# Performance work log

Hardware: AMD Instinct MI355X
Metric: run time of the kernel (lower is better)

Reference implementation:

```python
import jax, jax.numpy as jnp
import numpy as np

B, C, H, W = 64, 512, 7, 7        # x4: dim_b=512, layer4 spatial 7x7
HY, WY = 28, 28                   # y (x1): layer1 56x56 -> cov1 stride2 -> 28x28
NUM_HEADS = 8
HEAD_DIM = C // NUM_HEADS
SCALE = HEAD_DIM ** -0.5
K1, K2 = 2, 3
LN_EPS = 1e-5


def _avgpool_same(y, k, p):
    # torch nn.AvgPool2d(kernel=k, stride=1, padding=p), count_include_pad=True
    s = jax.lax.reduce_window(y, 0.0, jax.lax.add, (1, 1, k, k), (1, 1, 1, 1),
                              [(0, 0), (0, 0), (p, p), (p, p)])
    return s / float(k * k)


def setup_inputs() -> dict:
    key = jax.random.key(0)
    ks = jax.random.split(key, 8)
    x = jax.random.normal(ks[0], (B, C, H, W), dtype=jnp.float32)
    y = jax.random.normal(ks[1], (B, C, HY, WY), dtype=jnp.float32)
    # Linear weights stored as [in, out] (apply via x @ W)
    Wq = jax.random.normal(ks[2], (C, C), dtype=jnp.float32) * 0.02
    Wkv = jax.random.normal(ks[3], (C, 2 * C), dtype=jnp.float32) * 0.02
    Wproj = jax.random.normal(ks[4], (C, C), dtype=jnp.float32) * 0.02
    bproj = jnp.zeros((C,), dtype=jnp.float32)
    gamma = jnp.ones((C,), dtype=jnp.float32)
    beta = jnp.zeros((C,), dtype=jnp.float32)
    attn_w1 = jnp.full((1,), 0.5, dtype=jnp.float32)
    attn_w2 = jnp.full((1,), 0.5, dtype=jnp.float32)
    return dict(x=x, y=y, Wq=Wq, Wkv=Wkv, Wproj=Wproj, bproj=bproj,
                gamma=gamma, beta=beta, attn_w1=attn_w1, attn_w2=attn_w2)


def _topk_masked_softmax(attn, kc):
    # torch: scatter top-kc indices into a 0/1 mask, then where(mask>0, attn, -inf).
    # Equivalent (tie-free, as with continuous random logits): keep entries >= kth value.
    thr = jax.lax.top_k(attn, kc)[0][..., -1:]
    masked = jnp.where(attn >= jax.lax.stop_gradient(thr), attn, -jnp.inf)
    return jax.nn.softmax(masked, axis=-1)


def reference(x, y, Wq, Wkv, Wproj, bproj, gamma, beta, attn_w1, attn_w2):
    # Multi-scale pooling on y (all stride 1, 'same' spatial size)
    y = _avgpool_same(y, 3, 1) + _avgpool_same(y, 5, 2) + _avgpool_same(y, 7, 3)
    N1 = HY * WY
    y = y.reshape(B, C, N1).transpose(0, 2, 1)          # [B, N1, C]
    # LayerNorm over C
    mu = jnp.mean(y, axis=-1, keepdims=True)
    var = jnp.var(y, axis=-1, keepdims=True)
    y = (y - mu) / jnp.sqrt(var + LN_EPS) * gamma + beta

    N = H * W
    xs = x.reshape(B, C, N).transpose(0, 2, 1)          # [B, N, C]

    kv = (y @ Wkv).reshape(B, N1, 2, NUM_HEADS, HEAD_DIM)
    kv = kv.transpose(2, 0, 3, 1, 4)                    # [2, B, h, N1, d]
    k, v = kv[0], kv[1]
    q = (xs @ Wq).reshape(B, N, NUM_HEADS, HEAD_DIM).transpose(0, 2, 1, 3)  # [B,h,N,d]

    attn = jnp.einsum('bhnd,bhmd->bhnm', q, k) * SCALE  # [B, h, N, N1]

    attn1 = _topk_masked_softmax(attn, N1 // K1)
    attn2 = _topk_masked_softmax(attn, N1 // K2)
    out1 = jnp.einsum('bhnm,bhmd->bhnd', attn1, v)
    out2 = jnp.einsum('bhnm,bhmd->bhnd', attn2, v)
    out = out1 * attn_w1 + out2 * attn_w2               # [B, h, N, d]

    out = out.transpose(0, 2, 1, 3).reshape(B, N, C)    # [B, N, C]
    out = out @ Wproj + bproj
    return out.transpose(0, 2, 1).reshape(B, C, H, W)
```

## Files before the change

### kernel.cpp

```cpp
#include <hip/hip_runtime.h>
#include <hip/hip_bf16.h>


typedef __hip_bfloat16 bf16;
using bf16x8 = __attribute__((ext_vector_type(8))) short;
using f32x4 = __attribute__((ext_vector_type(4))) float;

#define DI __device__ __forceinline__

DI unsigned short b2u(float f) {
  bf16 h = __float2bfloat16(f);
  return *reinterpret_cast<unsigned short*>(&h);
}
DI float u2f(short s) { return __uint_as_float(((unsigned int)(unsigned short)s) << 16); }

DI float unkey(unsigned int k) {
  unsigned int u = (k & 0x80000000u) ? (k & 0x7FFFFFFFu) : ~k;
  return __uint_as_float(u);
}

__global__ __launch_bounds__(256) void pool2t_kernel(const float* __restrict__ y,
                                                     bf16* __restrict__ pooledT) {
  const int b = blockIdx.x >> 6, cg = blockIdx.x & 63;
  const float* src = y + ((size_t)b * 512 + cg * 8) * 784;
  bf16* drow = pooledT + ((size_t)b * 784) * 512 + cg * 8;
  __shared__ float I[8][870];
  const int tid = threadIdx.x;
  for (int i = tid; i < 6272; i += 256) {
    int p = i / 784, j = i - p * 784;
    int r = j / 28, c = j - r * 28;
    I[p][(r + 1) * 30 + c + 1] = src[p * 784 + j];
  }
  for (int i = tid; i < 8 * 58; i += 256) {
    int p = i / 58, e = i - p * 58;
    if (e < 30) I[p][e] = 0.f;
    else I[p][(e - 29) * 30] = 0.f;
  }
  __syncthreads();
  if (tid < 224) {
    int p = tid / 28, r = tid - (tid / 28) * 28;
    float run = 0.f;
    float* row = &I[p][(r + 1) * 30 + 1];
#pragma unroll
    for (int c = 0; c < 28; ++c) { run += row[c]; row[c] = run; }
  }
  __syncthreads();
  if (tid < 224) {
    int p = tid / 28, c = tid - (tid / 28) * 28;
    float run = 0.f;
    float* col = &I[p][30 + c + 1];
#pragma unroll
    for (int r = 0; r < 28; ++r) { run += col[r * 30]; col[r * 30] = run; }
  }
  __syncthreads();
  for (int j = tid; j < 784; j += 256) {
    int r = j / 28, c = j - (j / 28) * 28;
    int r0[3], r1[3], c0[3], c1[3];
#pragma unroll
    for (int pk = 1; pk <= 3; ++pk) {
      r0[pk - 1] = max(r - pk, 0) * 30;
      r1[pk - 1] = (min(r + pk, 27) + 1) * 30;
      c0[pk - 1] = max(c - pk, 0);
      c1[pk - 1] = min(c + pk, 27) + 1;
    }
    unsigned int u[4];
#pragma unroll
    for (int q = 0; q < 4; ++q) {
      float vv[2];
#pragma unroll
      for (int t = 0; t < 2; ++t) {
        const float* Ip = I[q * 2 + t];
        float acc = 0.f;
#pragma unroll
        for (int k = 0; k < 3; ++k) {
          float s = Ip[r1[k] + c1[k]] - Ip[r0[k] + c1[k]] - Ip[r1[k] + c0[k]] + Ip[r0[k] + c0[k]];
          acc += s * ((k == 0) ? (1.f / 9.f) : (k == 1) ? (1.f / 25.f) : (1.f / 49.f));
        }
        vv[t] = acc;
      }
      u[q] = (unsigned int)b2u(vv[0]) | ((unsigned int)b2u(vv[1]) << 16);
    }
    *reinterpret_cast<uint4*>(drow + (size_t)j * 512) = make_uint4(u[0], u[1], u[2], u[3]);
  }
}

__global__ __launch_bounds__(256) void lnrow_kernel(const bf16* __restrict__ pooledT,
                                                    const float* __restrict__ gamma,
                                                    const float* __restrict__ beta,
                                                    bf16* __restrict__ yln) {
  const int row = blockIdx.x * 4 + (threadIdx.x >> 6);
  const int lane = threadIdx.x & 63;
  bf16x8 raw = *reinterpret_cast<const bf16x8*>(pooledT + (size_t)row * 512 + lane * 8);
  float v[8];
  float s = 0.f, s2 = 0.f;
#pragma unroll
  for (int j = 0; j < 8; ++j) {
    v[j] = u2f(raw[j]);
    s += v[j];
    s2 += v[j] * v[j];
  }
#pragma unroll
  for (int off = 32; off; off >>= 1) {
    s += __shfl_xor(s, off, 64);
    s2 += __shfl_xor(s2, off, 64);
  }
  float mu = s * (1.f / 512.f);
  float rs = rsqrtf(s2 * (1.f / 512.f) - mu * mu + 1e-5f);
  float4 g0 = *reinterpret_cast<const float4*>(gamma + lane * 8);
  float4 g1 = *reinterpret_cast<const float4*>(gamma + lane * 8 + 4);
  float4 e0 = *reinterpret_cast<const float4*>(beta + lane * 8);
  float4 e1 = *reinterpret_cast<const float4*>(beta + lane * 8 + 4);
  float gg[8] = {g0.x, g0.y, g0.z, g0.w, g1.x, g1.y, g1.z, g1.w};
  float bb[8] = {e0.x, e0.y, e0.z, e0.w, e1.x, e1.y, e1.z, e1.w};
  unsigned int u[4];
#pragma unroll
  for (int q = 0; q < 4; ++q) {
    float o0 = (v[2 * q] - mu) * rs * gg[2 * q] + bb[2 * q];
    float o1 = (v[2 * q + 1] - mu) * rs * gg[2 * q + 1] + bb[2 * q + 1];
    u[q] = (unsigned int)b2u(o0) | ((unsigned int)b2u(o1) << 16);
  }
  *reinterpret_cast<uint4*>(yln + (size_t)row * 512 + lane * 8) = make_uint4(u[0], u[1], u[2], u[3]);
}

__global__ __launch_bounds__(256) void xst_kernel(const float* __restrict__ x,
                                                  bf16* __restrict__ xsTb) {
  int idx = blockIdx.x * 256 + threadIdx.x;
  int c = idx & 511;
  int rem = idx >> 9;
  int r = rem % 49, b = rem / 49;
  xsTb[idx] = __float2bfloat16(x[((size_t)b * 512 + c) * 49 + r]);
}

__global__ __launch_bounds__(256) void wt_kernel(const float* __restrict__ W,
                                                 bf16* __restrict__ WT, int N) {
  __shared__ float t[32][33];
  const int n0 = blockIdx.x * 32, k0 = blockIdx.y * 32;
  for (int i = threadIdx.x; i < 1024; i += 256) {
    int kr = i >> 5, nc = i & 31;
    t[kr][nc] = W[(size_t)(k0 + kr) * N + n0 + nc];
  }
  __syncthreads();
  for (int i = threadIdx.x; i < 1024; i += 256) {
    int nr = i >> 5, kc = i & 31;
    WT[(size_t)(n0 + nr) * 512 + k0 + kc] = __float2bfloat16(t[kc][nr]);
  }
}

__global__ __launch_bounds__(256) void vtpad_kernel(bf16* __restrict__ Vt) {
  int idx = blockIdx.x * 256 + threadIdx.x;
  int row = idx >> 4, c = idx & 15;
  Vt[(size_t)row * 800 + 784 + c] = __float2bfloat16(0.f);
}

#define GLD_LDS16(g, l)                                                              \
  __builtin_amdgcn_global_load_lds((const __attribute__((address_space(1))) unsigned int*)(g), \
                                   (__attribute__((address_space(3))) unsigned int*)(l), 16, 0, 0)

__global__ __launch_bounds__(256) void kv_mfma(const bf16* __restrict__ A,
                                               const bf16* __restrict__ Bt,
                                               bf16* __restrict__ Kb, bf16* __restrict__ Vt) {
  extern __shared__ __align__(16) bf16 smem[];
  bf16* As = smem;
  bf16* Bs = smem + 128 * 32;
  const int tid = threadIdx.x;
  const int lane = tid & 63;
  const int w = tid >> 6, wr = w >> 1, wc = w & 1;

  const int lin = blockIdx.y * 8 + blockIdx.x;
  const int c8 = lin & 7, j = lin >> 3;
  const int ex = j & 7, ey = c8 * 49 + (j >> 3);
  const int m0 = ey * 128, n0 = ex * 128;

  f32x4 acc[4][4];
#pragma unroll
  for (int m = 0; m < 4; ++m)
#pragma unroll
    for (int n = 0; n < 4; ++n) acc[m][n] = f32x4{0.f, 0.f, 0.f, 0.f};

  const int s0 = tid, s1 = tid + 256;
  const bf16* Ag0 = A + (size_t)(m0 + (s0 >> 2)) * 512 + (s0 & 3) * 8;
  const bf16* Ag1 = A + (size_t)(m0 + (s1 >> 2)) * 512 + (s1 & 3) * 8;
  const bf16* Bg0 = Bt + (size_t)(n0 + (s0 >> 2)) * 512 + (s0 & 3) * 8;
  const bf16* Bg1 = Bt + (size_t)(n0 + (s1 >> 2)) * 512 + (s1 & 3) * 8;
  bf16* Al0 = As + s0 * 8;
  bf16* Al1 = As + s1 * 8;
  bf16* Bl0 = Bs + s0 * 8;
  bf16* Bl1 = Bs + s1 * 8;

  const int fr = lane & 15;
  const int ko = (lane >> 4) * 8;
  const int rh = lane >> 4;

  for (int k0 = 0; k0 < 512; k0 += 32) {
    GLD_LDS16(Ag0 + k0, Al0);
    GLD_LDS16(Ag1 + k0, Al1);
    GLD_LDS16(Bg0 + k0, Bl0);
    GLD_LDS16(Bg1 + k0, Bl1);
    __syncthreads();
    bf16x8 af[4], bfr[4];
#pragma unroll
    for (int m = 0; m < 4; ++m)
      af[m] = *reinterpret_cast<const bf16x8*>(As + (wr * 64 + m * 16 + fr) * 32 + ko);
#pragma unroll
    for (int n = 0; n < 4; ++n)
      bfr[n] = *reinterpret_cast<const bf16x8*>(Bs + (wc * 64 + n * 16 + fr) * 32 + ko);
#pragma unroll
    for (int m = 0; m < 4; ++m)
#pragma unroll
      for (int n = 0; n < 4; ++n)
        acc[m][n] = __builtin_amdgcn_mfma_f32_16x16x32_bf16(af[m], bfr[n], acc[m][n], 0, 0, 0);
    __syncthreads();
  }

  if (n0 < 512) {
#pragma unroll
    for (int m = 0; m < 4; ++m) {
#pragma unroll
      for (int n = 0; n < 4; ++n) {
        int col = n0 + wc * 64 + n * 16 + fr;
        const size_t cbase = ((size_t)(col >> 6)) * (784 * 64) + (col & 63);
#pragma unroll
        for (int r = 0; r < 4; ++r) {
          int row = m0 + wr * 64 + m * 16 + rh * 4 + r;
          int b = row / 784, n1 = row - (row / 784) * 784;
          Kb[((size_t)b * 8) * (784 * 64) + cbase + (size_t)n1 * 64] = __float2bfloat16(acc[m][n][r]);
        }
      }
    }
  } else {
    bf16* stage = smem;
#pragma unroll
    for (int p = 0; p < 2; ++p) {
      __syncthreads();
      if (wr == p) {
#pragma unroll
        for (int m = 0; m < 4; ++m) {
#pragma unroll
          for (int n = 0; n < 4; ++n) {
            int coll = wc * 64 + n * 16 + fr;
            int rowl = m * 16 + rh * 4;
            unsigned int u0 = (unsigned int)b2u(acc[m][n][0]) | ((unsigned int)b2u(acc[m][n][1]) << 16);
            unsigned int u1 = (unsigned int)b2u(acc[m][n][2]) | ((unsigned int)b2u(acc[m][n][3]) << 16);
            *reinterpret_cast<uint2*>(stage + coll * 72 + rowl) = make_uint2(u0, u1);
          }
        }
      }
      __syncthreads();
      const int rbase = m0 + p * 64;
      for (int i = tid; i < 1024; i += 256) {
        int cc = i >> 3, tc = i & 7;
        int colg = n0 + cc;
        int h = (colg >> 6) & 7, d = colg & 63;
        int rs = rbase + tc * 8;
        int b = rs / 784, n1 = rs - b * 784;
        bf16x8 val = *reinterpret_cast<const bf16x8*>(stage + cc * 72 + tc * 8);
        bf16* dst = Vt + (((size_t)b * 8 + h) * 64 + d) * 800 + n1;
        if (n1 <= 776) {
          *reinterpret_cast<bf16x8*>(dst) = val;
        } else {
#pragma unroll
          for (int jj = 0; jj < 8; ++jj) {
            int rr = rs + jj;
            int bb2 = rr / 784, nn1 = rr - bb2 * 784;
            bf16 hv;
            *reinterpret_cast<short*>(&hv) = val[jj];
            Vt[(((size_t)bb2 * 8 + h) * 64 + d) * 800 + nn1] = hv;
          }
        }
      }
    }
  }
}

__global__ __launch_bounds__(256) void q_mfma(const bf16* __restrict__ A,
                                              const bf16* __restrict__ Bt,
                                              bf16* __restrict__ Qb) {
  __shared__ __align__(16) bf16 As[128 * 32];
  __shared__ __align__(16) bf16 Bs[128 * 32];
  const int tid = threadIdx.x;
  const int lane = tid & 63;
  const int w = tid >> 6, wr = w >> 1, wc = w & 1;
  const int m0 = blockIdx.y * 128, n0 = blockIdx.x * 128;

  f32x4 acc[4][4];
#pragma unroll
  for (int m = 0; m < 4; ++m)
#pragma unroll
    for (int n = 0; n < 4; ++n) acc[m][n] = f32x4{0.f, 0.f, 0.f, 0.f};

  const int s0 = tid, s1 = tid + 256;
  const bf16* Ag0 = A + (size_t)(m0 + (s0 >> 2)) * 512 + (s0 & 3) * 8;
  const bf16* Ag1 = A + (size_t)(m0 + (s1 >> 2)) * 512 + (s1 & 3) * 8;
  const bf16* Bg0 = Bt + (size_t)(n0 + (s0 >> 2)) * 512 + (s0 & 3) * 8;
  const bf16* Bg1 = Bt + (size_t)(n0 + (s1 >> 2)) * 512 + (s1 & 3) * 8;
  bf16* Al0 = As + s0 * 8;
  bf16* Al1 = As + s1 * 8;
  bf16* Bl0 = Bs + s0 * 8;
  bf16* Bl1 = Bs + s1 * 8;

  const int fr = lane & 15;
  const int ko = (lane >> 4) * 8;
  const int rh = lane >> 4;

  for (int k0 = 0; k0 < 512; k0 += 32) {
    GLD_LDS16(Ag0 + k0, Al0);
    GLD_LDS16(Ag1 + k0, Al1);
    GLD_LDS16(Bg0 + k0, Bl0);
    GLD_LDS16(Bg1 + k0, Bl1);
    __syncthreads();
    bf16x8 af[4], bfr[4];
#pragma unroll
    for (int m = 0; m < 4; ++m)
      af[m] = *reinterpret_cast<const bf16x8*>(As + (wr * 64 + m * 16 + fr) * 32 + ko);
#pragma unroll
    for (int n = 0; n < 4; ++n)
      bfr[n] = *reinterpret_cast<const bf16x8*>(Bs + (wc * 64 + n * 16 + fr) * 32 + ko);
#pragma unroll
    for (int m = 0; m < 4; ++m)
#pragma unroll
      for (int n = 0; n < 4; ++n)
        acc[m][n] = __builtin_amdgcn_mfma_f32_16x16x32_bf16(af[m], bfr[n], acc[m][n], 0, 0, 0);
    __syncthreads();
  }

#pragma unroll
  for (int m = 0; m < 4; ++m) {
#pragma unroll
    for (int n = 0; n < 4; ++n) {
      int col = n0 + wc * 64 + n * 16 + fr;
      const size_t cbase = ((size_t)(col >> 6)) * (49 * 64) + (col & 63);
#pragma unroll
      for (int r = 0; r < 4; ++r) {
        int row = m0 + wr * 64 + m * 16 + rh * 4 + r;
        if (row < 3136) {
          int b = row / 49, rr = row - (row / 49) * 49;
          Qb[((size_t)b * 8) * (49 * 64) + cbase + (size_t)rr * 64] = __float2bfloat16(acc[m][n][r]);
        }
      }
    }
  }
}

__global__ __launch_bounds__(256) void proj_mfma(const bf16* __restrict__ A,
                                                 const bf16* __restrict__ Bt,
                                                 const float* __restrict__ bias,
                                                 float* __restrict__ out) {
  __shared__ __align__(16) bf16 As[128 * 32];
  __shared__ __align__(16) bf16 Bs[128 * 32];
  const int tid = threadIdx.x;
  const int lane = tid & 63;
  const int w = tid >> 6, wr = w >> 1, wc = w & 1;
  const int m0 = blockIdx.y * 128, n0 = blockIdx.x * 128;

  f32x4 acc[4][4];
#pragma unroll
  for (int m = 0; m < 4; ++m)
#pragma unroll
    for (int n = 0; n < 4; ++n) acc[m][n] = f32x4{0.f, 0.f, 0.f, 0.f};

  const int s0 = tid, s1 = tid + 256;
  const bf16* Ag0 = A + (size_t)(m0 + (s0 >> 2)) * 1024 + (s0 & 3) * 8;
  const bf16* Ag1 = A + (size_t)(m0 + (s1 >> 2)) * 1024 + (s1 & 3) * 8;
  const bf16* Bg0 = Bt + (size_t)(n0 + (s0 >> 2)) * 512 + (s0 & 3) * 8;
  const bf16* Bg1 = Bt + (size_t)(n0 + (s1 >> 2)) * 512 + (s1 & 3) * 8;
  bf16* Al0 = As + s0 * 8;
  bf16* Al1 = As + s1 * 8;
  bf16* Bl0 = Bs + s0 * 8;
  bf16* Bl1 = Bs + s1 * 8;

  const int fr = lane & 15;
  const int ko = (lane >> 4) * 8;
  const int rh = lane >> 4;

  for (int k0 = 0; k0 < 1024; k0 += 32) {
    GLD_LDS16(Ag0 + k0, Al0);
    GLD_LDS16(Ag1 + k0, Al1);
    GLD_LDS16(Bg0 + (k0 & 511), Bl0);
    GLD_LDS16(Bg1 + (k0 & 511), Bl1);
    __syncthreads();
    bf16x8 af[4], bfr[4];
#pragma unroll
    for (int m = 0; m < 4; ++m)
      af[m] = *reinterpret_cast<const bf16x8*>(As + (wr * 64 + m * 16 + fr) * 32 + ko);
#pragma unroll
    for (int n = 0; n < 4; ++n)
      bfr[n] = *reinterpret_cast<const bf16x8*>(Bs + (wc * 64 + n * 16 + fr) * 32 + ko);
#pragma unroll
    for (int m = 0; m < 4; ++m)
#pragma unroll
      for (int n = 0; n < 4; ++n)
        acc[m][n] = __builtin_amdgcn_mfma_f32_16x16x32_bf16(af[m], bfr[n], acc[m][n], 0, 0, 0);
    __syncthreads();
  }

#pragma unroll
  for (int m = 0; m < 4; ++m) {
#pragma unroll
    for (int n = 0; n < 4; ++n) {
      int col = n0 + wc * 64 + n * 16 + fr;
      float bv = bias[col];
#pragma unroll
      for (int r = 0; r < 4; ++r) {
        int row = m0 + wr * 64 + m * 16 + rh * 4 + r;
        if (row < 3136) {
          int b = row / 49, rr = row - (row / 49) * 49;
          out[((size_t)b * 512 + col) * 49 + rr] = acc[m][n][r] + bv;
        }
      }
    }
  }
}

__global__ __launch_bounds__(256, 6) void attn_kernel(const bf16* __restrict__ Qb,
                                                      const bf16* __restrict__ K,
                                                      const bf16* __restrict__ Vt,
                                                      const float* __restrict__ aw1p,
                                                      const float* __restrict__ aw2p,
                                                      bf16* __restrict__ aoutHL) {
  const int lin = blockIdx.x;
  const int wk = (lin & 7) * 448 + (lin >> 3);
  const int bh = wk / 7;
  const int chunk = wk - bh * 7;
  const int b = bh >> 3, h = bh & 7;
  const int r0 = chunk * 7;
  const int tid = threadIdx.x;
  const int lane = tid & 63, w = tid >> 6;
  __shared__ __align__(16) bf16 sQb[16][72];
  __shared__ __align__(16) unsigned char sMem[21952];
  float* sLog = reinterpret_cast<float*>(sMem);
  bf16* sW = reinterpret_cast<bf16*>(sMem);

  const bf16* Qp = Qb + ((size_t)bh * 49 + r0) * 64;
  for (int i = tid; i < 1024; i += 256) {
    int r = i >> 6, d = i & 63;
    sQb[r][d] = (r < 7) ? Qp[r * 64 + d] : __float2bfloat16(0.f);
  }
  __syncthreads();

  const bf16* Kp = K + (size_t)bh * (784 * 64);
  const int fr = lane & 15, ko = (lane >> 4) * 8, rh = lane >> 4;
  {
    const bf16x8 aq0 = *reinterpret_cast<const bf16x8*>(&sQb[fr][ko]);
    const bf16x8 aq1 = *reinterpret_cast<const bf16x8*>(&sQb[fr][32 + ko]);
    const int rbase = rh * 4;
    const bf16* kbase = Kp + (size_t)fr * 64 + ko;
    bf16x8 kq0[4], kq1[4];
#pragma unroll
    for (int s = 0; s < 4; ++s) {
      int nt = w + s * 4;
      int ntc = nt < 49 ? nt : 48;
      const bf16* kr = kbase + (size_t)ntc * 1024;
      kq0[s] = *reinterpret_cast<const bf16x8*>(kr);
      kq1[s] = *reinterpret_cast<const bf16x8*>(kr + 32);
    }
#pragma unroll
    for (int i = 0; i < 13; ++i) {
      const int s = i & 3;
      const int nt = w + i * 4;
      if (nt < 49) {
        f32x4 acc = {0.f, 0.f, 0.f, 0.f};
        acc = __builtin_amdgcn_mfma_f32_16x16x32_bf16(aq0, kq0[s], acc, 0, 0, 0);
        acc = __builtin_amdgcn_mfma_f32_16x16x32_bf16(aq1, kq1[s], acc, 0, 0, 0);
#pragma unroll
        for (int r = 0; r < 4; ++r) {
          int row = rbase + r;
          if (row < 7) sLog[row * 784 + nt * 16 + fr] = acc[r] * 0.125f;
        }
      }
      const int ntn = w + (i + 4) * 4;
      if (ntn < 49) {
        const bf16* kr = kbase + (size_t)ntn * 1024;
        kq0[s] = *reinterpret_cast<const bf16x8*>(kr);
        kq1[s] = *reinterpret_cast<const bf16x8*>(kr + 32);
      }
    }
  }
  __syncthreads();

  const int ra = w;
  const int rb = (w + 4 < 7) ? (w + 4) : w;
  float va[13], vb[13];
#pragma unroll
  for (int i = 0; i < 13; ++i) {
    int m = lane + i * 64;
    va[i] = (m < 784) ? sLog[ra * 784 + m] : -INFINITY;
    vb[i] = (m < 784) ? sLog[rb * 784 + m] : -INFINITY;
  }
  __syncthreads();

  float mxa = va[0], mxb = vb[0];
#pragma unroll
  for (int i = 1; i < 13; ++i) {
    mxa = fmaxf(mxa, va[i]);
    mxb = fmaxf(mxb, vb[i]);
  }
#pragma unroll
  for (int off = 32; off; off >>= 1) {
    mxa = fmaxf(mxa, __shfl_xor(mxa, off, 64));
    mxb = fmaxf(mxb, __shfl_xor(mxb, off, 64));
  }

  unsigned int t1a = 0u, t2a = 0u, t1b = 0u, t2b = 0u;
  bool d1a = false, d2a = false, d1b = false, d2b = false;
  for (int bit = 31; bit >= 0; --bit) {
    const unsigned int mb = 1u << bit;
    if (!d1a) {
      float cf = unkey(t1a | mb);
      int n = 0;
#pragma unroll
      for (int i = 0; i < 13; ++i) n += __popcll(__ballot(va[i] >= cf));
      if (n >= 392) { t1a |= mb; d1a = (n == 392); }
    }
    if (!d2a) {
      float cf = unkey(t2a | mb);
      int n = 0;
#pragma unroll
      for (int i = 0; i < 13; ++i) n += __popcll(__ballot(va[i] >= cf));
      if (n >= 261) { t2a |= mb; d2a = (n == 261); }
    }
    if (!d1b) {
      float cf = unkey(t1b | mb);
      int n = 0;
#pragma unroll
      for (int i = 0; i < 13; ++i) n += __popcll(__ballot(vb[i] >= cf));
      if (n >= 392) { t1b |= mb; d1b = (n == 392); }
    }
    if (!d2b) {
      float cf = unkey(t2b | mb);
      int n = 0;
#pragma unroll
      for (int i = 0; i < 13; ++i) n += __popcll(__ballot(vb[i] >= cf));
      if (n >= 261) { t2b |= mb; d2b = (n == 261); }
    }
    if (d1a & d2a & d1b & d2b) break;
  }
  const float T1a = unkey(t1a), T2a = unkey(t2a);
  const float T1b = unkey(t1b), T2b = unkey(t2b);

  const float aw1 = aw1p[0], aw2 = aw2p[0];
  float ea[13], eb[13];
  float z1a = 0.f, z2a = 0.f, z1b = 0.f, z2b = 0.f;
#pragma unroll
  for (int i = 0; i < 13; ++i) {
    ea[i] = __expf(va[i] - mxa);
    eb[i] = __expf(vb[i] - mxb);
    if (va[i] >= T1a) z1a += ea[i];
    if (va[i] >= T2a) z2a += ea[i];
    if (vb[i] >= T1b) z1b += eb[i];
    if (vb[i] >= T2b) z2b += eb[i];
  }
#pragma unroll
  for (int off = 32; off; off >>= 1) {
    z1a += __shfl_xor(z1a, off, 64);
    z2a += __shfl_xor(z2a, off, 64);
    z1b += __shfl_xor(z1b, off, 64);
    z2b += __shfl_xor(z2b, off, 64);
  }
  const float a1a = aw1 / z1a, a2a = aw2 / z2a;
  const float a1b = aw1 / z1b, a2b = aw2 / z2b;
#pragma unroll
  for (int i = 0; i < 13; ++i) {
    int m = lane + i * 64;
    if (m < 784) {
      float wa = ea[i] * (((va[i] >= T1a) ? a1a : 0.f) + ((va[i] >= T2a) ? a2a : 0.f));
      sW[ra * 808 + m] = __float2bfloat16(wa);
      float wb = eb[i] * (((vb[i] >= T1b) ? a1b : 0.f) + ((vb[i] >= T2b) ? a2b : 0.f));
      sW[rb * 808 + m] = __float2bfloat16(wb);
    }
  }
  if (lane < 16) {
    sW[ra * 808 + 784 + lane] = __float2bfloat16(0.f);
    sW[rb * 808 + 784 + lane] = __float2bfloat16(0.f);
  }
  if (w == 3)
    for (int i = lane; i < 808; i += 64) sW[7 * 808 + i] = __float2bfloat16(0.f);

  const bf16* vbase = Vt + ((size_t)bh * 64 + w * 16 + fr) * 800;
  bf16x8 vq[4];
#pragma unroll
  for (int s = 0; s < 4; ++s)
    vq[s] = *reinterpret_cast<const bf16x8*>(vbase + s * 32 + ko);
  __syncthreads();

  const bf16* wrow = sW + (fr < 7 ? fr : 7) * 808;
  f32x4 acc0 = {0.f, 0.f, 0.f, 0.f}, acc1 = {0.f, 0.f, 0.f, 0.f};
#pragma unroll
  for (int ks = 0; ks < 25; ++ks) {
    const int s = ks & 3;
    bf16x8 a = *reinterpret_cast<const bf16x8*>(wrow + ks * 32 + ko);
    if (ks & 1)
      acc1 = __builtin_amdgcn_mfma_f32_16x16x32_bf16(a, vq[s], acc1, 0, 0, 0);
    else
      acc0 = __builtin_amdgcn_mfma_f32_16x16x32_bf16(a, vq[s], acc0, 0, 0, 0);
    if (ks + 4 < 25)
      vq[s] = *reinterpret_cast<const bf16x8*>(vbase + (ks + 4) * 32 + ko);
  }
  acc0 += acc1;
#pragma unroll
  for (int r = 0; r < 4; ++r) {
    int row = rh * 4 + r;
    if (row < 7) {
      float v = acc0[r];
      bf16 hi = __float2bfloat16(v);
      bf16 lo = __float2bfloat16(v - __bfloat162float(hi));
      size_t base = ((size_t)(b * 49 + r0 + row)) * 1024 + h * 64 + w * 16 + fr;
      aoutHL[base] = hi;
      aoutHL[base + 512] = lo;
    }
  }
}

extern "C" void kernel_launch(void* const* d_in, const int* in_sizes, int n_in, void* d_out,
                              int out_size, void* d_ws, size_t ws_size, hipStream_t stream) {
  const float* x = (const float*)d_in[0];
  const float* y = (const float*)d_in[1];
  const float* Wq = (const float*)d_in[2];
  const float* Wkv = (const float*)d_in[3];
  const float* Wproj = (const float*)d_in[4];
  const float* bproj = (const float*)d_in[5];
  const float* gamma = (const float*)d_in[6];
  const float* beta = (const float*)d_in[7];
  const float* aw1 = (const float*)d_in[8];
  const float* aw2 = (const float*)d_in[9];
  float* out = (float*)d_out;

  char* w = (char*)d_ws;
  const size_t SZ = 51380224ull;
  const size_t SZV = 52428800ull;
  bf16* pooledT = (bf16*)(w);
  bf16* yln = (bf16*)(w + SZ);
  bf16* Kb = (bf16*)(w);
  bf16* Vt = (bf16*)(w + 2 * SZ);
  size_t off = 2 * SZ + SZV;
  bf16* xsTb = (bf16*)(w + off);    off += 3276800;
  bf16* Qb = (bf16*)(w + off);      off += 3276800;
  bf16* aoutHL = (bf16*)(w + off);  off += 6553600;
  bf16* wkvT = (bf16*)(w + off);    off += 1048576;
  bf16* wqT = (bf16*)(w + off);     off += 524288;
  bf16* wpT = (bf16*)(w + off);     off += 524288;

  wt_kernel<<<dim3(32, 16), dim3(256), 0, stream>>>(Wkv, wkvT, 1024);
  wt_kernel<<<dim3(16, 16), dim3(256), 0, stream>>>(Wq, wqT, 512);
  wt_kernel<<<dim3(16, 16), dim3(256), 0, stream>>>(Wproj, wpT, 512);
  pool2t_kernel<<<dim3(4096), dim3(256), 0, stream>>>(y, pooledT);
  vtpad_kernel<<<dim3(2048), dim3(256), 0, stream>>>(Vt);
  lnrow_kernel<<<dim3(12544), dim3(256), 0, stream>>>(pooledT, gamma, beta, yln);
  xst_kernel<<<dim3(6272), dim3(256), 0, stream>>>(x, xsTb);
  q_mfma<<<dim3(4, 25), dim3(256), 0, stream>>>(xsTb, wqT, Qb);
  kv_mfma<<<dim3(8, 392), dim3(256), 18432, stream>>>(yln, wkvT, Kb, Vt);
  attn_kernel<<<dim3(3584), dim3(256), 0, stream>>>(Qb, Kb, Vt, aw1, aw2, aoutHL);
  proj_mfma<<<dim3(4, 25), dim3(256), 0, stream>>>(aoutHL, wpT, bproj, out);
}
```

Baseline: 346.2 us.

## Merge prep kernels, load Q directly to registers, raise attn occupancy

Folds the three weight-transpose launches, the x transpose and the V padding kernel into a single prep_kernel that dispatches work by block index, cutting launch count. In the attention kernel, Q fragments are now read straight from global memory into registers, which drops the shared-memory staging buffer and one barrier. The zeroing of the unused eighth weight row is also removed, since that row only feeds output rows that are thrown away. Launch bounds rise from 6 to 7 blocks per SIMD target, which could force register spills.

```diff
diff --git a/kernel.cpp b/kernel.cpp
--- a/kernel.cpp
+++ b/kernel.cpp
@@ -122,34 +122,44 @@
   *reinterpret_cast<uint4*>(yln + (size_t)row * 512 + lane * 8) = make_uint4(u[0], u[1], u[2], u[3]);
 }
 
-__global__ __launch_bounds__(256) void xst_kernel(const float* __restrict__ x,
-                                                  bf16* __restrict__ xsTb) {
-  int idx = blockIdx.x * 256 + threadIdx.x;
-  int c = idx & 511;
-  int rem = idx >> 9;
-  int r = rem % 49, b = rem / 49;
-  xsTb[idx] = __float2bfloat16(x[((size_t)b * 512 + c) * 49 + r]);
-}
-
-__global__ __launch_bounds__(256) void wt_kernel(const float* __restrict__ W,
-                                                 bf16* __restrict__ WT, int N) {
+__global__ __launch_bounds__(256) void prep_kernel(const float* __restrict__ Wkv,
+                                                   const float* __restrict__ Wq,
+                                                   const float* __restrict__ Wproj,
+                                                   const float* __restrict__ x,
+                                                   bf16* __restrict__ wkvT, bf16* __restrict__ wqT,
+                                                   bf16* __restrict__ wpT, bf16* __restrict__ xsTb,
+                                                   bf16* __restrict__ Vt) {
   __shared__ float t[32][33];
-  const int n0 = blockIdx.x * 32, k0 = blockIdx.y * 32;
-  for (int i = threadIdx.x; i < 1024; i += 256) {
-    int kr = i >> 5, nc = i & 31;
-    t[kr][nc] = W[(size_t)(k0 + kr) * N + n0 + nc];
-  }
-  __syncthreads();
-  for (int i = threadIdx.x; i < 1024; i += 256) {
-    int nr = i >> 5, kc = i & 31;
-    WT[(size_t)(n0 + nr) * 512 + k0 + kc] = __float2bfloat16(t[kc][nr]);
-  }
-}
-
-__global__ __launch_bounds__(256) void vtpad_kernel(bf16* __restrict__ Vt) {
-  int idx = blockIdx.x * 256 + threadIdx.x;
-  int row = idx >> 4, c = idx & 15;
-  Vt[(size_t)row * 800 + 784 + c] = __float2bfloat16(0.f);
+  const int blk = blockIdx.x;
+  const int tid = threadIdx.x;
+  if (blk < 1024) {
+    const float* W;
+    bf16* WT;
+    int N, bx, by;
+    if (blk < 512) { W = Wkv; WT = wkvT; N = 1024; bx = blk & 31; by = blk >> 5; }
+    else if (blk < 768) { W = Wq; WT = wqT; N = 512; bx = (blk - 512) & 15; by = (blk - 512) >> 4; }
+    else { W = Wproj; WT = wpT; N = 512; bx = (blk - 768) & 15; by = (blk - 768) >> 4; }
+    const int n0 = bx * 32, k0 = by * 32;
+    for (int i = tid; i < 1024; i += 256) {
+      int kr = i >> 5, nc = i & 31;
+      t[kr][nc] = W[(size_t)(k0 + kr) * N + n0 + nc];
+    }
+    __syncthreads();
+    for (int i = tid; i < 1024; i += 256) {
+      int nr = i >> 5, kc = i & 31;
+      WT[(size_t)(n0 + nr) * 512 + k0 + kc] = __float2bfloat16(t[kc][nr]);
+    }
+  } else if (blk < 7296) {
+    int idx = (blk - 1024) * 256 + tid;
+    int c = idx & 511;
+    int rem = idx >> 9;
+    int r = rem % 49, b = rem / 49;
+    xsTb[idx] = __float2bfloat16(x[((size_t)b * 512 + c) * 49 + r]);
+  } else {
+    int idx = (blk - 7296) * 256 + tid;
+    int row = idx >> 4, c = idx & 15;
+    Vt[(size_t)row * 800 + 784 + c] = __float2bfloat16(0.f);
+  }
 }
 
 #define GLD_LDS16(g, l)                                                              \
@@ -411,7 +421,7 @@
   }
 }
 
-__global__ __launch_bounds__(256, 6) void attn_kernel(const bf16* __restrict__ Qb,
+__global__ __launch_bounds__(256, 7) void attn_kernel(const bf16* __restrict__ Qb,
                                                       const bf16* __restrict__ K,
                                                       const bf16* __restrict__ Vt,
                                                       const float* __restrict__ aw1p,
@@ -425,23 +435,19 @@
   const int r0 = chunk * 7;
   const int tid = threadIdx.x;
   const int lane = tid & 63, w = tid >> 6;
-  __shared__ __align__(16) bf16 sQb[16][72];
   __shared__ __align__(16) unsigned char sMem[21952];
   float* sLog = reinterpret_cast<float*>(sMem);
   bf16* sW = reinterpret_cast<bf16*>(sMem);
 
+  const int fr = lane & 15, ko = (lane >> 4) * 8, rh = lane >> 4;
+
   const bf16* Qp = Qb + ((size_t)bh * 49 + r0) * 64;
-  for (int i = tid; i < 1024; i += 256) {
-    int r = i >> 6, d = i & 63;
-    sQb[r][d] = (r < 7) ? Qp[r * 64 + d] : __float2bfloat16(0.f);
-  }
-  __syncthreads();
+  const int qrow = (fr < 7) ? fr : 6;
+  const bf16x8 aq0 = *reinterpret_cast<const bf16x8*>(Qp + qrow * 64 + ko);
+  const bf16x8 aq1 = *reinterpret_cast<const bf16x8*>(Qp + qrow * 64 + 32 + ko);
 
   const bf16* Kp = K + (size_t)bh * (784 * 64);
-  const int fr = lane & 15, ko = (lane >> 4) * 8, rh = lane >> 4;
   {
-    const bf16x8 aq0 = *reinterpret_cast<const bf16x8*>(&sQb[fr][ko]);
-    const bf16x8 aq1 = *reinterpret_cast<const bf16x8*>(&sQb[fr][32 + ko]);
     const int rbase = rh * 4;
     const bf16* kbase = Kp + (size_t)fr * 64 + ko;
     bf16x8 kq0[4], kq1[4];
@@ -572,8 +578,6 @@
     sW[ra * 808 + 784 + lane] = __float2bfloat16(0.f);
     sW[rb * 808 + 784 + lane] = __float2bfloat16(0.f);
   }
-  if (w == 3)
-    for (int i = lane; i < 808; i += 64) sW[7 * 808 + i] = __float2bfloat16(0.f);
 
   const bf16* vbase = Vt + ((size_t)bh * 64 + w * 16 + fr) * 800;
   bf16x8 vq[4];
@@ -582,7 +586,7 @@
     vq[s] = *reinterpret_cast<const bf16x8*>(vbase + s * 32 + ko);
   __syncthreads();
 
-  const bf16* wrow = sW + (fr < 7 ? fr : 7) * 808;
+  const bf16* wrow = sW + ((fr < 7) ? fr : 7) * 808;
   f32x4 acc0 = {0.f, 0.f, 0.f, 0.f}, acc1 = {0.f, 0.f, 0.f, 0.f};
 #pragma unroll
   for (int ks = 0; ks < 25; ++ks) {
@@ -639,13 +643,9 @@
   bf16* wqT = (bf16*)(w + off);     off += 524288;
   bf16* wpT = (bf16*)(w + off);     off += 524288;
 
-  wt_kernel<<<dim3(32, 16), dim3(256), 0, stream>>>(Wkv, wkvT, 1024);
-  wt_kernel<<<dim3(16, 16), dim3(256), 0, stream>>>(Wq, wqT, 512);
-  wt_kernel<<<dim3(16, 16), dim3(256), 0, stream>>>(Wproj, wpT, 512);
+  prep_kernel<<<dim3(9344), dim3(256), 0, stream>>>(Wkv, Wq, Wproj, x, wkvT, wqT, wpT, xsTb, Vt);
   pool2t_kernel<<<dim3(4096), dim3(256), 0, stream>>>(y, pooledT);
-  vtpad_kernel<<<dim3(2048), dim3(256), 0, stream>>>(Vt);
   lnrow_kernel<<<dim3(12544), dim3(256), 0, stream>>>(pooledT, gamma, beta, yln);
-  xst_kernel<<<dim3(6272), dim3(256), 0, stream>>>(x, xsTb);
   q_mfma<<<dim3(4, 25), dim3(256), 0, stream>>>(xsTb, wqT, Qb);
   kv_mfma<<<dim3(8, 392), dim3(256), 18432, stream>>>(yln, wkvT, Kb, Vt);
   attn_kernel<<<dim3(3584), dim3(256), 0, stream>>>(Qb, Kb, Vt, aw1, aw2, aoutHL);
```

Measured after the change: 327.7 us. 5.4% less time.
